# Kernel optimization log

Hardware: AMD Instinct MI355X
Metric: run time of the kernel (lower is better)

Reference implementation:

```python
import jax, jax.numpy as jnp
import numpy as np

G = 8192          # graphs in batch
A = 5             # num_agents (nodes per graph)
N = G * A         # total nodes
IN_CH = 29
HID = 64
HEADS = 8
D = HID * HEADS   # 512, node/graph feature dim
NOPT = 4
ADIM = 3


def _lin(key, fan_in, fan_out):
    return jax.random.normal(key, (fan_in, fan_out), jnp.float32) / np.sqrt(fan_in)


def setup_inputs() -> dict:
    key = jax.random.key(0)
    ks = jax.random.split(key, 40)
    # --- graph structure: G fully-connected 5-node graphs + self loops ---
    pairs = np.array([(i, j) for i in range(A) for j in range(A) if i != j])  # [20,2]
    base = (np.arange(G)[:, None] * A)
    src = (base + pairs[None, :, 0]).reshape(-1)
    dst = (base + pairs[None, :, 1]).reshape(-1)
    # GATConv adds self loops (fill_value=0.0 for edge_attr)
    loop = np.arange(N)
    edge_src = jnp.asarray(np.concatenate([src, loop]), jnp.int32)
    edge_dst = jnp.asarray(np.concatenate([dst, loop]), jnp.int32)
    e_real = jax.random.uniform(ks[0], (src.shape[0], 1), jnp.float32)
    edge_attr = jnp.concatenate([e_real, jnp.zeros((N, 1), jnp.float32)], axis=0)
    batch_map = jnp.asarray(np.repeat(np.arange(G), A), jnp.int32)
    x = jax.random.normal(ks[1], (N, IN_CH), jnp.float32)
    sc = 1.0 / np.sqrt(HID)
    inp = dict(
        x=x, edge_attr=edge_attr, edge_src=edge_src, edge_dst=edge_dst, batch_map=batch_map,
        # conv1
        W1=_lin(ks[2], IN_CH, D), as1=jax.random.normal(ks[3], (HEADS, HID)) * sc,
        ad1=jax.random.normal(ks[4], (HEADS, HID)) * sc, We1=_lin(ks[5], 1, D),
        ae1=jax.random.normal(ks[6], (HEADS, HID)) * sc, b1=jnp.zeros((D,), jnp.float32),
        # conv2
        W2=_lin(ks[7], D, D), as2=jax.random.normal(ks[8], (HEADS, HID)) * sc,
        ad2=jax.random.normal(ks[9], (HEADS, HID)) * sc, We2=_lin(ks[10], 1, D),
        ae2=jax.random.normal(ks[11], (HEADS, HID)) * sc, b2=jnp.zeros((D,), jnp.float32),
        # policy-over-options head
        pw1=_lin(ks[12], D, 2 * HID), pb1=jnp.zeros((2 * HID,)), pw2=_lin(ks[13], 2 * HID, NOPT), pb2=jnp.zeros((NOPT,)),
        # q-options head
        qw1=_lin(ks[14], D, 2 * HID), qb1=jnp.zeros((2 * HID,)), qw2=_lin(ks[15], 2 * HID, NOPT), qb2=jnp.zeros((NOPT,)),
        # intra-option actor head (option 0), input dim = node + graph feature = 2*D
        aw1=_lin(ks[16], 2 * D, 2 * HID), ab1=jnp.zeros((2 * HID,)), aw2=_lin(ks[17], 2 * HID, 2 * ADIM), ab2=jnp.zeros((2 * ADIM,)),
        # termination head (option 0)
        tw1=_lin(ks[18], D, HID), tb1=jnp.zeros((HID,)), tw2=_lin(ks[19], HID, 1), tb2=jnp.zeros((1,)),
        action_limits=jnp.array([1.0, 1.0, 3.14159], jnp.float32),
    )
    return inp


def _gat(x, src, dst, eattr, W, a_s, a_d, We, a_e, b):
    n = x.shape[0]
    h = (x @ W).reshape(n, HEADS, HID)                      # [N,H,C]
    e = (eattr @ We).reshape(-1, HEADS, HID)                # [E,H,C]
    lg = ((h * a_s).sum(-1)[src] + (h * a_d).sum(-1)[dst]
          + (e * a_e).sum(-1))                              # [E,H]
    lg = jnp.where(lg > 0, lg, 0.2 * lg)                    # leaky_relu(0.2)
    m = jax.ops.segment_max(lg, dst, num_segments=n)
    p = jnp.exp(lg - m[dst])
    denom = jax.ops.segment_sum(p, dst, num_segments=n)[dst] + 1e-16
    alpha = p / denom                                       # scatter-softmax over dst
    out = jax.ops.segment_sum(alpha[:, :, None] * h[src], dst, num_segments=n)
    return out.reshape(n, HEADS * HID) + b


def reference(x, edge_attr, edge_src, edge_dst, batch_map,
              W1, as1, ad1, We1, ae1, b1,
              W2, as2, ad2, We2, ae2, b2,
              pw1, pb1, pw2, pb2, qw1, qb1, qw2, qb2,
              aw1, ab1, aw2, ab2, tw1, tb1, tw2, tb2, action_limits):
    h = jax.nn.relu(_gat(x, edge_src, edge_dst, edge_attr, W1, as1, ad1, We1, ae1, b1))
    h = jax.nn.relu(_gat(h, edge_src, edge_dst, edge_attr, W2, as2, ad2, We2, ae2, b2))
    # global_mean_pool
    cnt = jax.ops.segment_sum(jnp.ones((h.shape[0],), h.dtype), batch_map, num_segments=G)
    g = jax.ops.segment_sum(h, batch_map, num_segments=G) / cnt[:, None]   # [G,D]
    pi = jax.nn.relu(g @ pw1 + pb1) @ pw2 + pb2                            # [G,NOPT]
    q = jax.nn.relu(g @ qw1 + qb1) @ qw2 + qb2                             # [G,NOPT]
    term = jax.nn.sigmoid(jax.nn.relu(g @ tw1 + tb1) @ tw2 + tb2)          # [G,1]
    # per-graph first num_agents nodes == all nodes here (5 per graph)
    agent = h.reshape(G, A, D)
    comb = jnp.concatenate([agent, jnp.broadcast_to(g[:, None, :], (G, A, D))], axis=-1)
    ho = jax.nn.relu(comb @ aw1 + ab1) @ aw2 + ab2                          # [G,A,6]
    mean_raw, log_std_raw = jnp.split(ho, 2, axis=-1)
    mean = jnp.tanh(mean_raw) * action_limits                               # [G,A,3]
    std = 0.05 + jax.nn.sigmoid(log_std_raw) * 0.45 + 1e-6
    return jnp.concatenate([pi, q, term, mean.reshape(G, -1), std.reshape(G, -1)], axis=1)
```

## Files before the change

### kernel.cpp

```cpp
#include <hip/hip_runtime.h>
#include <hip/hip_bf16.h>
#include <math.h>

#define GG 8192
#define AA 5
#define NN (GG * AA)
#define DD 512

typedef unsigned short ushort_t;
typedef unsigned int uint_t;

__device__ inline float bf2f(ushort_t u) {
  union { uint_t i; float f; } c; c.i = ((uint_t)u) << 16; return c.f;
}
__device__ inline ushort_t f2bf(float f) {
  union { float f; uint_t i; } c; c.f = f;
  uint_t r = c.i + 0x7fffu + ((c.i >> 16) & 1u);
  return (ushort_t)(r >> 16);
}

using frag8 = __attribute__((ext_vector_type(8))) short;
using f32x4 = __attribute__((ext_vector_type(4))) float;

typedef __attribute__((address_space(3))) void lds_void;
typedef __attribute__((address_space(1))) const void gbl_void;
#define GLL(g, l) __builtin_amdgcn_global_load_lds((gbl_void*)(g), (lds_void*)(l), 16, 0, 0)

__device__ inline int xcd_swz(int bid, int nwg) {
  return (bid & 7) * (nwg >> 3) + (bid >> 3);
}

__global__ __launch_bounds__(256) void k_prep(
    const float* __restrict__ x, const float* __restrict__ W1,
    const float* __restrict__ W2, const float* __restrict__ pw1,
    const float* __restrict__ qw1, const float* __restrict__ tw1,
    const float* __restrict__ aw1, const float* __restrict__ pb1,
    const float* __restrict__ qb1, const float* __restrict__ tb1,
    const float* __restrict__ ab1, const float* __restrict__ We1,
    const float* __restrict__ ae1, const float* __restrict__ We2,
    const float* __restrict__ ae2, const float* __restrict__ as1,
    const float* __restrict__ ad1, const float* __restrict__ as2,
    const float* __restrict__ ad2, const float* __restrict__ pw2,
    const float* __restrict__ pb2, const float* __restrict__ qw2,
    const float* __restrict__ qb2, const float* __restrict__ tw2,
    const float* __restrict__ tb2, const float* __restrict__ aw2,
    const float* __restrict__ ab2, ushort_t* __restrict__ xpad32,
    ushort_t* __restrict__ W1T32, ushort_t* __restrict__ W2T,
    ushort_t* __restrict__ WcatT, ushort_t* __restrict__ aw1topT,
    ushort_t* __restrict__ wsc1T, ushort_t* __restrict__ wsc2T,
    float* __restrict__ bcat, float* __restrict__ sce,
    float* __restrict__ woutT, float* __restrict__ bout) {
  int b = blockIdx.x;
  int t = threadIdx.x;
  if (b < 1024) {
    int i = b * 256 + t;
    int n = i >> 9, k = i & 511;
    W2T[(size_t)n * 512 + k] = f2bf(W2[(size_t)k * 512 + n]);
    float v;
    if (n < 128)      v = pw1[(size_t)k * 128 + n];
    else if (n < 256) v = qw1[(size_t)k * 128 + (n - 128)];
    else if (n < 320) v = tw1[(size_t)k * 64 + (n - 256)];
    else if (n < 448) v = aw1[(size_t)(512 + k) * 128 + (n - 320)];
    else              v = 0.f;
    WcatT[(size_t)n * 512 + k] = f2bf(v);
    if (n < 128) aw1topT[(size_t)n * 512 + k] = f2bf(aw1[(size_t)k * 128 + n]);
    if (k == 0) {
      float bv;
      if (n < 128)      bv = pb1[n];
      else if (n < 256) bv = qb1[n - 128];
      else if (n < 320) bv = tb1[n - 256];
      else if (n < 448) bv = ab1[n - 320];
      else              bv = 0.f;
      bcat[n] = bv;
    }
    if (i < 512 * 32) {
      int nn = i >> 5, kk = i & 31;
      W1T32[i] = (kk < 29) ? f2bf(W1[(size_t)kk * 512 + nn]) : (ushort_t)0;
    }
    if (i < 8192) {
      int k2 = i & 511, s = i >> 9;
      int head = s >> 1;
      const float* av = ((s & 1) ? ad2 : as2) + head * 64;
      const float* wr = W2 + (size_t)k2 * 512 + head * 64;
      float val = 0.f;
      for (int c = 0; c < 64; ++c) val = fmaf(wr[c], av[c], val);
      wsc2T[i] = f2bf(val);
    }
    if (i < 512) {
      int k1 = i & 31, s = i >> 5;
      int head = s >> 1;
      float val = 0.f;
      if (k1 < 29) {
        const float* av = ((s & 1) ? ad1 : as1) + head * 64;
        const float* wr = W1 + (size_t)k1 * 512 + head * 64;
        for (int c = 0; c < 64; ++c) val = fmaf(wr[c], av[c], val);
      }
      wsc1T[i] = f2bf(val);
    }
    if (i < 16) {
      int h = i & 7;
      const float* Wp = (i < 8) ? We1 : We2;
      const float* ap = (i < 8) ? ae1 : ae2;
      float c = 0.f;
      for (int k2 = 0; k2 < 64; ++k2) c = fmaf(Wp[h * 64 + k2], ap[h * 64 + k2], c);
      sce[i] = c;
    }
    if (i < 5120) {
      int j = i / 40, o = i % 40;
      float wv;
      if (o < 4)       wv = pw2[j * 4 + o];
      else if (o < 8)  wv = qw2[j * 4 + (o - 4)];
      else if (o == 8) wv = (j < 64) ? tw2[j] : 0.f;
      else if (o < 24) wv = aw2[j * 6 + (o - 9) % 3];
      else if (o < 39) wv = aw2[j * 6 + 3 + (o - 24) % 3];
      else             wv = 0.f;
      woutT[i] = wv;
      if (j == 0) {
        float bv;
        if (o < 4)       bv = pb2[o];
        else if (o < 8)  bv = qb2[o - 4];
        else if (o == 8) bv = tb2[0];
        else if (o < 24) bv = ab2[(o - 9) % 3];
        else if (o < 39) bv = ab2[3 + (o - 24) % 3];
        else             bv = 0.f;
        bout[o] = bv;
      }
    }
  } else {
    int i = (b - 1024) * 256 + t;
    int n = i >> 5, k = i & 31;
    xpad32[i] = (k < 29) ? f2bf(x[(size_t)n * 29 + k]) : (ushort_t)0;
  }
}

__global__ __launch_bounds__(1024) void k_mega(
    const ushort_t* __restrict__ xpad32, const ushort_t* __restrict__ W1T32,
    const ushort_t* __restrict__ wsc1T, const ushort_t* __restrict__ W2T,
    const ushort_t* __restrict__ wsc2T, const float* __restrict__ eattr,
    const float* __restrict__ sce, const float* __restrict__ b1,
    const float* __restrict__ b2, ushort_t* __restrict__ h2,
    ushort_t* __restrict__ gmean) {
  __shared__ __align__(16) char smem[149504];
  const int t = threadIdx.x;
  const int lane = t & 63;
  const int w = t >> 6;
  const int l15 = lane & 15;
  const int ko2 = ((((lane >> 4) ^ (lane & 3) ^ ((lane >> 2) & 3)) & 3) * 16);
  int lid = xcd_swz(blockIdx.x, gridDim.x);
  const int m0 = lid * 80;
  const int g0 = lid * 16;
  ushort_t* h1buf = (ushort_t*)smem;
  float* sal = (float*)(smem + 124160);
  float* sss = (float*)(smem + 136960);
  float* ssd = (float*)(smem + 139520);
  const f32x4 zz = {0.f, 0.f, 0.f, 0.f};
  f32x4 acc[5][2], asc[5];
#pragma unroll
  for (int mt = 0; mt < 5; ++mt) { acc[mt][0] = zz; acc[mt][1] = zz; asc[mt] = zz; }

  {
#pragma unroll
    for (int r_ = 0; r_ < 2; ++r_) {
      int c_ = t + r_ * 1024; int row_ = c_ >> 2;
      int sw_ = ((((c_ & 3) ^ (row_ & 3) ^ ((row_ >> 2) & 3)) & 3)) * 8;
      GLL(W1T32 + (size_t)row_ * 32 + sw_, smem + 81920 + c_ * 16);
    }
    if (t < 320) {
      int c_ = t; int row_ = c_ >> 2;
      int sw_ = ((((c_ & 3) ^ (row_ & 3) ^ ((row_ >> 2) & 3)) & 3)) * 8;
      GLL(xpad32 + (size_t)(m0 + row_) * 32 + sw_, smem + 114688 + c_ * 16);
    } else if (t < 384) {
      int c_ = t - 320; int row_ = c_ >> 2;
      int sw_ = ((((c_ & 3) ^ (row_ & 3) ^ ((row_ >> 2) & 3)) & 3)) * 8;
      GLL(wsc1T + (size_t)row_ * 32 + sw_, smem + 119808 + c_ * 16);
    }
  }
  asm volatile("s_waitcnt vmcnt(0)" ::: "memory");
  __builtin_amdgcn_s_barrier();
  {
    const char* bb = smem + 81920;
    const char* aa = smem + 114688;
    const char* sb = smem + 119808;
    frag8 af[5], bfr[2];
#pragma unroll
    for (int mt = 0; mt < 5; ++mt)
      af[mt] = *(const frag8*)(aa + (mt * 16 + l15) * 64 + ko2);
#pragma unroll
    for (int n = 0; n < 2; ++n)
      bfr[n] = *(const frag8*)(bb + ((2 * w + n) * 16 + l15) * 64 + ko2);
#pragma unroll
    for (int mt = 0; mt < 5; ++mt)
#pragma unroll
      for (int n = 0; n < 2; ++n)
        acc[mt][n] = __builtin_amdgcn_mfma_f32_16x16x32_bf16(af[mt], bfr[n], acc[mt][n], 0, 0, 0);
    if (w == 15) {
      frag8 sfr = *(const frag8*)(sb + l15 * 64 + ko2);
#pragma unroll
      for (int mt = 0; mt < 5; ++mt)
        asc[mt] = __builtin_amdgcn_mfma_f32_16x16x32_bf16(af[mt], sfr, asc[mt], 0, 0, 0);
    }
  }
  if (w == 15) {
    float* dst = (l15 & 1) ? ssd : sss;
    int hd = l15 >> 1;
    int q4 = (lane >> 4) * 4;
#pragma unroll
    for (int mt = 0; mt < 5; ++mt)
#pragma unroll
      for (int r = 0; r < 4; ++r)
        dst[(mt * 16 + q4 + r) * 8 + hd] = asc[mt][r];
  }
  __syncthreads();
  if (t < 640) {
    int gi = t / 40, jh = t % 40;
    int j = jh >> 3, hd = jh & 7;
    int g = g0 + gi;
    float sdj = ssd[(gi * 5 + j) * 8 + hd];
    float ce = sce[hd];
    float lg[5], mx = -1e30f;
#pragma unroll
    for (int i = 0; i < 5; ++i) {
      float l = sss[(gi * 5 + i) * 8 + hd] + sdj;
      if (i != j) l = fmaf(eattr[(size_t)g * 20 + i * 4 + (j > i ? j - 1 : j)], ce, l);
      l = l > 0.f ? l : 0.2f * l;
      lg[i] = l; mx = fmaxf(mx, l);
    }
    float s = 0.f;
#pragma unroll
    for (int i = 0; i < 5; ++i) { lg[i] = __expf(lg[i] - mx); s += lg[i]; }
    float inv = 1.f / (s + 1e-16f);
#pragma unroll
    for (int i = 0; i < 5; ++i) sal[((gi * 5 + j) * 5 + i) * 8 + hd] = lg[i] * inv;
  }
  __syncthreads();
  {
    float* hbf = (float*)(smem + 81920);
#pragma unroll
    for (int p = 0; p < 4; ++p) {
      if ((w >> 2) == p) {
        int q4 = (lane >> 4) * 4;
#pragma unroll
        for (int mt = 0; mt < 5; ++mt)
#pragma unroll
          for (int n = 0; n < 2; ++n) {
            int lc = (w & 3) * 32 + n * 16 + l15;
#pragma unroll
            for (int r = 0; r < 4; ++r)
              hbf[(mt * 16 + q4 + r) * 132 + lc] = acc[mt][n][r];
          }
      }
      __syncthreads();
      if (t < 512) {
        int gi = t >> 5, cq = t & 31;
        int hd = 2 * p + (cq >> 4);
        int cg = p * 128 + cq * 4;
        float hv[5][4];
#pragma unroll
        for (int i = 0; i < 5; ++i)
          *(float4*)hv[i] = *(const float4*)&hbf[(gi * 5 + i) * 132 + cq * 4];
        float4 bb4 = *(const float4*)&b1[cg];
        int chunk = cg >> 5, slot = (cg >> 3) & 3, boff = (cg & 7) * 2;
#pragma unroll
        for (int j = 0; j < 5; ++j) {
          float o0 = bb4.x, o1 = bb4.y, o2 = bb4.z, o3 = bb4.w;
#pragma unroll
          for (int i = 0; i < 5; ++i) {
            float a = sal[((gi * 5 + j) * 5 + i) * 8 + hd];
            o0 = fmaf(a, hv[i][0], o0); o1 = fmaf(a, hv[i][1], o1);
            o2 = fmaf(a, hv[i][2], o2); o3 = fmaf(a, hv[i][3], o3);
          }
          o0 = fmaxf(o0, 0.f); o1 = fmaxf(o1, 0.f);
          o2 = fmaxf(o2, 0.f); o3 = fmaxf(o3, 0.f);
          uint2 wv_;
          wv_.x = (uint_t)f2bf(o0) | ((uint_t)f2bf(o1) << 16);
          wv_.y = (uint_t)f2bf(o2) | ((uint_t)f2bf(o3) << 16);
          int row = gi * 5 + j;
          int phys = slot ^ (row & 3) ^ ((row >> 2) & 3);
          *(uint2*)((char*)h1buf + chunk * 5120 + row * 64 + phys * 16 + boff) = wv_;
        }
      }
      __syncthreads();
    }
  }

#pragma unroll
  for (int mt = 0; mt < 5; ++mt) { acc[mt][0] = zz; acc[mt][1] = zz; asc[mt] = zz; }
#define FS2(bi, kk0)                                                           \
  {                                                                            \
    char* bb_ = smem + 81920 + (bi) * 32768;                                   \
    char* sb_ = smem + 147456 + (bi) * 1024;                                   \
    _Pragma("unroll")                                                          \
    for (int r_ = 0; r_ < 2; ++r_) {                                           \
      int c_ = t + r_ * 1024; int row_ = c_ >> 2;                              \
      int sw_ = ((((c_ & 3) ^ (row_ & 3) ^ ((row_ >> 2) & 3)) & 3)) * 8;       \
      GLL(W2T + (size_t)row_ * 512 + (kk0) + sw_, bb_ + c_ * 16);              \
    }                                                                          \
    if (t < 64) {                                                              \
      int c_ = t; int row_ = c_ >> 2;                                          \
      int sw_ = ((((c_ & 3) ^ (row_ & 3) ^ ((row_ >> 2) & 3)) & 3)) * 8;       \
      GLL(wsc2T + (size_t)row_ * 512 + (kk0) + sw_, sb_ + c_ * 16);            \
    }                                                                          \
  }
  FS2(0, 0);
  asm volatile("s_waitcnt vmcnt(0)" ::: "memory");
  __builtin_amdgcn_s_barrier();
  for (int ts = 0; ts < 16; ++ts) {
    int cur = ts & 1;
    if (ts + 1 < 16) FS2(cur ^ 1, (ts + 1) * 32);
    const char* bb = smem + 81920 + cur * 32768;
    const char* aa = (const char*)h1buf + ts * 5120;
    const char* sb = smem + 147456 + cur * 1024;
    frag8 af[5], bfr[2];
#pragma unroll
    for (int mt = 0; mt < 5; ++mt)
      af[mt] = *(const frag8*)(aa + (mt * 16 + l15) * 64 + ko2);
#pragma unroll
    for (int n = 0; n < 2; ++n)
      bfr[n] = *(const frag8*)(bb + ((2 * w + n) * 16 + l15) * 64 + ko2);
    __builtin_amdgcn_s_setprio(1);
#pragma unroll
    for (int mt = 0; mt < 5; ++mt)
#pragma unroll
      for (int n = 0; n < 2; ++n)
        acc[mt][n] = __builtin_amdgcn_mfma_f32_16x16x32_bf16(af[mt], bfr[n], acc[mt][n], 0, 0, 0);
    if (w == 15) {
      frag8 sfr = *(const frag8*)(sb + l15 * 64 + ko2);
#pragma unroll
      for (int mt = 0; mt < 5; ++mt)
        asc[mt] = __builtin_amdgcn_mfma_f32_16x16x32_bf16(af[mt], sfr, asc[mt], 0, 0, 0);
    }
    __builtin_amdgcn_s_setprio(0);
    __builtin_amdgcn_sched_barrier(0);
    asm volatile("s_waitcnt vmcnt(0)" ::: "memory");
    __builtin_amdgcn_s_barrier();
  }
#undef FS2
  if (w == 15) {
    float* dst = (l15 & 1) ? ssd : sss;
    int hd = l15 >> 1;
    int q4 = (lane >> 4) * 4;
#pragma unroll
    for (int mt = 0; mt < 5; ++mt)
#pragma unroll
      for (int r = 0; r < 4; ++r)
        dst[(mt * 16 + q4 + r) * 8 + hd] = asc[mt][r];
  }
  __syncthreads();
  if (t < 640) {
    int gi = t / 40, jh = t % 40;
    int j = jh >> 3, hd = jh & 7;
    int g = g0 + gi;
    float sdj = ssd[(gi * 5 + j) * 8 + hd];
    float ce = sce[8 + hd];
    float lg[5], mx = -1e30f;
#pragma unroll
    for (int i = 0; i < 5; ++i) {
      float l = sss[(gi * 5 + i) * 8 + hd] + sdj;
      if (i != j) l = fmaf(eattr[(size_t)g * 20 + i * 4 + (j > i ? j - 1 : j)], ce, l);
      l = l > 0.f ? l : 0.2f * l;
      lg[i] = l; mx = fmaxf(mx, l);
    }
    float s = 0.f;
#pragma unroll
    for (int i = 0; i < 5; ++i) { lg[i] = __expf(lg[i] - mx); s += lg[i]; }
    float inv = 1.f / (s + 1e-16f);
#pragma unroll
    for (int i = 0; i < 5; ++i) sal[((gi * 5 + j) * 5 + i) * 8 + hd] = lg[i] * inv;
  }
  __syncthreads();
  {
    float* hbf = (float*)(smem + 81920);
#pragma unroll
    for (int p = 0; p < 4; ++p) {
      if ((w >> 2) == p) {
        int q4 = (lane >> 4) * 4;
#pragma unroll
        for (int mt = 0; mt < 5; ++mt)
#pragma unroll
          for (int n = 0; n < 2; ++n) {
            int lc = (w & 3) * 32 + n * 16 + l15;
#pragma unroll
            for (int r = 0; r < 4; ++r)
              hbf[(mt * 16 + q4 + r) * 132 + lc] = acc[mt][n][r];
          }
      }
      __syncthreads();
      if (t < 512) {
        int gi = t >> 5, cq = t & 31;
        int hd = 2 * p + (cq >> 4);
        int cg = p * 128 + cq * 4;
        float hv[5][4];
#pragma unroll
        for (int i = 0; i < 5; ++i)
          *(float4*)hv[i] = *(const float4*)&hbf[(gi * 5 + i) * 132 + cq * 4];
        float4 bb4 = *(const float4*)&b2[cg];
        float gs0 = 0.f, gs1 = 0.f, gs2 = 0.f, gs3 = 0.f;
#pragma unroll
        for (int j = 0; j < 5; ++j) {
          float o0 = bb4.x, o1 = bb4.y, o2 = bb4.z, o3 = bb4.w;
#pragma unroll
          for (int i = 0; i < 5; ++i) {
            float a = sal[((gi * 5 + j) * 5 + i) * 8 + hd];
            o0 = fmaf(a, hv[i][0], o0); o1 = fmaf(a, hv[i][1], o1);
            o2 = fmaf(a, hv[i][2], o2); o3 = fmaf(a, hv[i][3], o3);
          }
          o0 = fmaxf(o0, 0.f); o1 = fmaxf(o1, 0.f);
          o2 = fmaxf(o2, 0.f); o3 = fmaxf(o3, 0.f);
          uint2 wv_;
          wv_.x = (uint_t)f2bf(o0) | ((uint_t)f2bf(o1) << 16);
          wv_.y = (uint_t)f2bf(o2) | ((uint_t)f2bf(o3) << 16);
          *(uint2*)(h2 + ((size_t)(g0 + gi) * 5 + j) * 512 + cg) = wv_;
          gs0 += o0; gs1 += o1; gs2 += o2; gs3 += o3;
        }
        uint2 wv_;
        wv_.x = (uint_t)f2bf(gs0 * 0.2f) | ((uint_t)f2bf(gs1 * 0.2f) << 16);
        wv_.y = (uint_t)f2bf(gs2 * 0.2f) | ((uint_t)f2bf(gs3 * 0.2f) << 16);
        *(uint2*)(gmean + (size_t)(g0 + gi) * 512 + cg) = wv_;
      }
      __syncthreads();
    }
  }
}

template <int EPI>
__device__ __forceinline__ void gemm_body(
    const ushort_t* __restrict__ A, const ushort_t* __restrict__ BT,
    const float* __restrict__ bias, ushort_t* __restrict__ Cv,
    int M, int N, int K, int m0, int n0, char* lds) {
  int t = threadIdx.x;
  int lane = t & 63;
  int wv = t >> 6;
  int wr = (wv >> 1) * 64, wc = (wv & 1) * 64;
  f32x4 acc[4][4] = {};
  int ch0 = t, ch1 = t + 256;
  int row0 = ch0 >> 2, row1 = ch1 >> 2;
  int sw0 = (((ch0 & 3) ^ (row0 & 3) ^ ((row0 >> 2) & 3)) & 3) * 8;
  int sw1 = (((ch1 & 3) ^ (row1 & 3) ^ ((row1 >> 2) & 3)) & 3) * 8;
  int ko2 = ((((lane >> 4) ^ (lane & 3) ^ ((lane >> 2) & 3)) & 3) * 16);
  const int nt = K >> 5;
#define STAGE(bi, kk0)                                                         \
  {                                                                            \
    char* ab = lds + (bi) * 16384;                                             \
    GLL(A + (size_t)(m0 + row0) * K + (kk0) + sw0, ab + ch0 * 16);             \
    GLL(A + (size_t)(m0 + row1) * K + (kk0) + sw1, ab + ch1 * 16);             \
    GLL(BT + (size_t)(n0 + row0) * K + (kk0) + sw0, ab + 8192 + ch0 * 16);     \
    GLL(BT + (size_t)(n0 + row1) * K + (kk0) + sw1, ab + 8192 + ch1 * 16);     \
  }
  STAGE(0, 0);
  asm volatile("s_waitcnt vmcnt(0)" ::: "memory");
  __builtin_amdgcn_s_barrier();
  for (int ts = 0; ts < nt; ++ts) {
    int cur = ts & 1;
    if (ts + 1 < nt) STAGE(cur ^ 1, (ts + 1) * 32);
    const char* ab = lds + cur * 16384;
    frag8 af[4], bfr[4];
#pragma unroll
    for (int m = 0; m < 4; ++m)
      af[m] = *(const frag8*)(ab + (wr + m * 16 + (lane & 15)) * 64 + ko2);
#pragma unroll
    for (int n = 0; n < 4; ++n)
      bfr[n] = *(const frag8*)(ab + 8192 + (wc + n * 16 + (lane & 15)) * 64 + ko2);
    __builtin_amdgcn_s_setprio(1);
#pragma unroll
    for (int m = 0; m < 4; ++m)
#pragma unroll
      for (int n = 0; n < 4; ++n)
        acc[m][n] = __builtin_amdgcn_mfma_f32_16x16x32_bf16(af[m], bfr[n], acc[m][n], 0, 0, 0);
    __builtin_amdgcn_s_setprio(0);
    __builtin_amdgcn_sched_barrier(0);
    asm volatile("s_waitcnt vmcnt(0)" ::: "memory");
    __builtin_amdgcn_s_barrier();
  }
#undef STAGE
  int r4 = (lane >> 4) * 4;
  int cl = lane & 15;
#pragma unroll
  for (int m = 0; m < 4; ++m) {
#pragma unroll
    for (int n = 0; n < 4; ++n) {
      int col = n0 + wc + n * 16 + cl;
      float bb = (EPI == 2) ? bias[col] : 0.f;
#pragma unroll
      for (int r = 0; r < 4; ++r) {
        int row = m0 + wr + m * 16 + r4 + r;
        float v = acc[m][n][r] + bb;
        if (EPI == 2 && col < 320) v = fmaxf(v, 0.f);
        Cv[(size_t)row * N + col] = f2bf(v);
      }
    }
  }
}

__global__ __launch_bounds__(256) void k_hgemm(
    const ushort_t* __restrict__ h2, const ushort_t* __restrict__ aw1topT,
    ushort_t* __restrict__ ahid, const ushort_t* __restrict__ gmean,
    const ushort_t* __restrict__ WcatT, const float* __restrict__ bcat,
    ushort_t* __restrict__ hcat) {
  __shared__ char lds[32768];
  int bid = blockIdx.x;
  if (bid < 320) {
    int lid = xcd_swz(bid, 320);
    gemm_body<1>(h2, aw1topT, nullptr, ahid, NN, 128, DD, lid * 128, 0, lds);
  } else {
    int lid = xcd_swz(bid - 320, 256);
    gemm_body<2>(gmean, WcatT, bcat, hcat, GG, DD, DD, (lid >> 2) * 128, (lid & 3) * 128, lds);
  }
}

__global__ __launch_bounds__(256) void k_heads(
    const ushort_t* __restrict__ hcat, const ushort_t* __restrict__ ahid,
    const float* __restrict__ woutT, const float* __restrict__ bout,
    const float* __restrict__ alim, float* __restrict__ out) {
  int g0 = blockIdx.x * 4;
  int t = threadIdx.x;
  __shared__ float sbuf[4224];
  for (int i = t; i < 4224; i += 256) {
    int gi = i / 1056, r = i - gi * 1056;
    const ushort_t* grow = hcat + (size_t)(g0 + gi) * 512;
    float v = 0.f;
    if (r < 128)                  v = bf2f(grow[r]);
    else if (r >= 132 && r < 260) v = bf2f(grow[128 + r - 132]);
    else if (r >= 264 && r < 328) v = bf2f(grow[256 + r - 264]);
    else if (r >= 396) {
      int q = r - 396; int a = q / 132; int j = q - a * 132;
      if (j < 128)
        v = fmaxf(bf2f(ahid[((size_t)(g0 + gi) * 5 + a) * 128 + j]) + bf2f(grow[320 + j]), 0.f);
    }
    sbuf[i] = v;
  }
  __syncthreads();
  int gi = t >> 6, o = t & 63;
  int oc = o < 39 ? o : 39;
  int seg;
  if (oc < 4)       seg = 0;
  else if (oc < 8)  seg = 132;
  else if (oc == 8) seg = 264;
  else {
    int idx = (oc < 24) ? oc - 9 : oc - 24;
    seg = 396 + (idx / 3) * 132;
  }
  const float* ip = &sbuf[gi * 1056 + seg];
  float a0 = 0.f, a1 = 0.f, a2 = 0.f, a3 = 0.f;
#pragma unroll
  for (int j = 0; j < 128; j += 4) {
    a0 = fmaf(ip[j + 0], woutT[(j + 0) * 40 + oc], a0);
    a1 = fmaf(ip[j + 1], woutT[(j + 1) * 40 + oc], a1);
    a2 = fmaf(ip[j + 2], woutT[(j + 2) * 40 + oc], a2);
    a3 = fmaf(ip[j + 3], woutT[(j + 3) * 40 + oc], a3);
  }
  float res = (a0 + a1) + (a2 + a3) + bout[oc];
  if (o < 39) {
    if (o == 8)       res = 1.f / (1.f + __expf(-res));
    else if (o >= 24) res = 0.05f + 0.45f / (1.f + __expf(-res)) + 1e-6f;
    else if (o >= 9)  res = tanhf(res) * alim[(o - 9) % 3];
    out[(size_t)(g0 + gi) * 39 + o] = res;
  }
}

extern "C" void kernel_launch(void* const* d_in, const int* in_sizes, int n_in,
                              void* d_out, int out_size, void* d_ws, size_t ws_size,
                              hipStream_t stream) {
  const float* x     = (const float*)d_in[0];
  const float* eattr = (const float*)d_in[1];
  const float* W1  = (const float*)d_in[5];
  const float* as1 = (const float*)d_in[6];
  const float* ad1 = (const float*)d_in[7];
  const float* We1 = (const float*)d_in[8];
  const float* ae1 = (const float*)d_in[9];
  const float* b1  = (const float*)d_in[10];
  const float* W2  = (const float*)d_in[11];
  const float* as2 = (const float*)d_in[12];
  const float* ad2 = (const float*)d_in[13];
  const float* We2 = (const float*)d_in[14];
  const float* ae2 = (const float*)d_in[15];
  const float* b2  = (const float*)d_in[16];
  const float* pw1 = (const float*)d_in[17];
  const float* pb1 = (const float*)d_in[18];
  const float* pw2 = (const float*)d_in[19];
  const float* pb2 = (const float*)d_in[20];
  const float* qw1 = (const float*)d_in[21];
  const float* qb1 = (const float*)d_in[22];
  const float* qw2 = (const float*)d_in[23];
  const float* qb2 = (const float*)d_in[24];
  const float* aw1 = (const float*)d_in[25];
  const float* ab1 = (const float*)d_in[26];
  const float* aw2 = (const float*)d_in[27];
  const float* ab2 = (const float*)d_in[28];
  const float* tw1 = (const float*)d_in[29];
  const float* tb1 = (const float*)d_in[30];
  const float* tw2 = (const float*)d_in[31];
  const float* tb2 = (const float*)d_in[32];
  const float* alim = (const float*)d_in[33];

  const size_t BIGE = (size_t)NN * DD;
  char* p = (char*)d_ws;
  ushort_t* h2     = (ushort_t*)p; p += BIGE * 2;
  ushort_t* gmean  = (ushort_t*)p; p += (size_t)GG * DD * 2;
  ushort_t* xpad32 = (ushort_t*)p; p += (size_t)NN * 32 * 2;
  ushort_t* W1T32  = (ushort_t*)p; p += (size_t)512 * 32 * 2;
  ushort_t* W2T    = (ushort_t*)p; p += (size_t)512 * 512 * 2;
  ushort_t* WcatT  = (ushort_t*)p; p += (size_t)512 * 512 * 2;
  ushort_t* aw1topT = (ushort_t*)p; p += (size_t)128 * 512 * 2;
  ushort_t* wsc1T  = (ushort_t*)p; p += (size_t)16 * 32 * 2;
  ushort_t* wsc2T  = (ushort_t*)p; p += (size_t)16 * 512 * 2;
  float* bcat  = (float*)p; p += 512 * 4;
  float* sce   = (float*)p; p += 16 * 4;
  float* woutT = (float*)p; p += 5120 * 4;
  float* bout  = (float*)p; p += 40 * 4;
  ushort_t* ahid = (ushort_t*)p; p += (size_t)NN * 128 * 2;
  ushort_t* hcat = (ushort_t*)p;

  k_prep<<<1024 + 5120, 256, 0, stream>>>(
      x, W1, W2, pw1, qw1, tw1, aw1, pb1, qb1, tb1, ab1,
      We1, ae1, We2, ae2, as1, ad1, as2, ad2,
      pw2, pb2, qw2, qb2, tw2, tb2, aw2, ab2,
      xpad32, W1T32, W2T, WcatT, aw1topT, wsc1T, wsc2T,
      bcat, sce, woutT, bout);
  k_mega<<<GG / 16, 1024, 0, stream>>>(
      xpad32, W1T32, wsc1T, W2T, wsc2T, eattr, sce, b1, b2, h2, gmean);
  k_hgemm<<<320 + 256, 256, 0, stream>>>(h2, aw1topT, ahid, gmean, WcatT, bcat, hcat);
  k_heads<<<GG / 4, 256, 0, stream>>>(hcat, ahid, woutT, bout, alim, (float*)d_out);
}
```

Measured before the change: 105.8 us.

## Fuse head GEMMs into mega kernel, keep h2 and gmean in LDS

The second-layer GAT output and per-graph mean now stay in shared memory instead of being written to global h2/gmean buffers. The actor-hidden GEMM (h2 × aw1top) and the concatenated head GEMM (gmean × Wcat) run inside k_mega on that on-chip data, and the separate k_hgemm launch is removed. This avoids a roughly 40 MB round trip through global memory plus one kernel launch. In exchange each block does extra small GEMMs with poorly shaped tiles (16-row gmean tile, uneven 3/2 m-tile split), restages the weights per block, and uses more LDS.

```diff
diff --git a/kernel.cpp b/kernel.cpp
--- a/kernel.cpp
+++ b/kernel.cpp
@@ -136,11 +136,12 @@
 __global__ __launch_bounds__(1024) void k_mega(
     const ushort_t* __restrict__ xpad32, const ushort_t* __restrict__ W1T32,
     const ushort_t* __restrict__ wsc1T, const ushort_t* __restrict__ W2T,
-    const ushort_t* __restrict__ wsc2T, const float* __restrict__ eattr,
-    const float* __restrict__ sce, const float* __restrict__ b1,
-    const float* __restrict__ b2, ushort_t* __restrict__ h2,
-    ushort_t* __restrict__ gmean) {
-  __shared__ __align__(16) char smem[149504];
+    const ushort_t* __restrict__ wsc2T, const ushort_t* __restrict__ aw1topT,
+    const ushort_t* __restrict__ WcatT, const float* __restrict__ bcat,
+    const float* __restrict__ eattr, const float* __restrict__ sce,
+    const float* __restrict__ b1, const float* __restrict__ b2,
+    ushort_t* __restrict__ ahid, ushort_t* __restrict__ hcat) {
+  __shared__ __align__(16) char smem[158720];
   const int t = threadIdx.x;
   const int lane = t & 63;
   const int w = t >> 6;
@@ -149,10 +150,11 @@
   int lid = xcd_swz(blockIdx.x, gridDim.x);
   const int m0 = lid * 80;
   const int g0 = lid * 16;
-  ushort_t* h1buf = (ushort_t*)smem;
+  ushort_t* hbuf = (ushort_t*)smem;
   float* sal = (float*)(smem + 124160);
   float* sss = (float*)(smem + 136960);
   float* ssd = (float*)(smem + 139520);
+  ushort_t* gmb = (ushort_t*)(smem + 142080);
   const f32x4 zz = {0.f, 0.f, 0.f, 0.f};
   f32x4 acc[5][2], asc[5];
 #pragma unroll
@@ -276,7 +278,7 @@
           wv_.y = (uint_t)f2bf(o2) | ((uint_t)f2bf(o3) << 16);
           int row = gi * 5 + j;
           int phys = slot ^ (row & 3) ^ ((row >> 2) & 3);
-          *(uint2*)((char*)h1buf + chunk * 5120 + row * 64 + phys * 16 + boff) = wv_;
+          *(uint2*)((char*)hbuf + chunk * 5120 + row * 64 + phys * 16 + boff) = wv_;
         }
       }
       __syncthreads();
@@ -308,7 +310,7 @@
     int cur = ts & 1;
     if (ts + 1 < 16) FS2(cur ^ 1, (ts + 1) * 32);
     const char* bb = smem + 81920 + cur * 32768;
-    const char* aa = (const char*)h1buf + ts * 5120;
+    const char* aa = (const char*)hbuf + ts * 5120;
     const char* sb = smem + 147456 + cur * 1024;
     frag8 af[5], bfr[2];
 #pragma unroll
@@ -394,6 +396,7 @@
         for (int i = 0; i < 5; ++i)
           *(float4*)hv[i] = *(const float4*)&hbf[(gi * 5 + i) * 132 + cq * 4];
         float4 bb4 = *(const float4*)&b2[cg];
+        int chunk = cg >> 5, slot = (cg >> 3) & 3, boff = (cg & 7) * 2;
         float gs0 = 0.f, gs1 = 0.f, gs2 = 0.f, gs3 = 0.f;
 #pragma unroll
         for (int j = 0; j < 5; ++j) {
@@ -409,101 +412,117 @@
           uint2 wv_;
           wv_.x = (uint_t)f2bf(o0) | ((uint_t)f2bf(o1) << 16);
           wv_.y = (uint_t)f2bf(o2) | ((uint_t)f2bf(o3) << 16);
-          *(uint2*)(h2 + ((size_t)(g0 + gi) * 5 + j) * 512 + cg) = wv_;
+          int row = gi * 5 + j;
+          int phys = slot ^ (row & 3) ^ ((row >> 2) & 3);
+          *(uint2*)((char*)hbuf + chunk * 5120 + row * 64 + phys * 16 + boff) = wv_;
           gs0 += o0; gs1 += o1; gs2 += o2; gs3 += o3;
         }
-        uint2 wv_;
-        wv_.x = (uint_t)f2bf(gs0 * 0.2f) | ((uint_t)f2bf(gs1 * 0.2f) << 16);
-        wv_.y = (uint_t)f2bf(gs2 * 0.2f) | ((uint_t)f2bf(gs3 * 0.2f) << 16);
-        *(uint2*)(gmean + (size_t)(g0 + gi) * 512 + cg) = wv_;
+        uint2 gv_;
+        gv_.x = (uint_t)f2bf(gs0 * 0.2f) | ((uint_t)f2bf(gs1 * 0.2f) << 16);
+        gv_.y = (uint_t)f2bf(gs2 * 0.2f) | ((uint_t)f2bf(gs3 * 0.2f) << 16);
+        *(uint2*)(gmb + (size_t)gi * 520 + cg) = gv_;
       }
       __syncthreads();
     }
   }
-}
-
-template <int EPI>
-__device__ __forceinline__ void gemm_body(
-    const ushort_t* __restrict__ A, const ushort_t* __restrict__ BT,
-    const float* __restrict__ bias, ushort_t* __restrict__ Cv,
-    int M, int N, int K, int m0, int n0, char* lds) {
-  int t = threadIdx.x;
-  int lane = t & 63;
-  int wv = t >> 6;
-  int wr = (wv >> 1) * 64, wc = (wv & 1) * 64;
-  f32x4 acc[4][4] = {};
-  int ch0 = t, ch1 = t + 256;
-  int row0 = ch0 >> 2, row1 = ch1 >> 2;
-  int sw0 = (((ch0 & 3) ^ (row0 & 3) ^ ((row0 >> 2) & 3)) & 3) * 8;
-  int sw1 = (((ch1 & 3) ^ (row1 & 3) ^ ((row1 >> 2) & 3)) & 3) * 8;
-  int ko2 = ((((lane >> 4) ^ (lane & 3) ^ ((lane >> 2) & 3)) & 3) * 16);
-  const int nt = K >> 5;
-#define STAGE(bi, kk0)                                                         \
-  {                                                                            \
-    char* ab = lds + (bi) * 16384;                                             \
-    GLL(A + (size_t)(m0 + row0) * K + (kk0) + sw0, ab + ch0 * 16);             \
-    GLL(A + (size_t)(m0 + row1) * K + (kk0) + sw1, ab + ch1 * 16);             \
-    GLL(BT + (size_t)(n0 + row0) * K + (kk0) + sw0, ab + 8192 + ch0 * 16);     \
-    GLL(BT + (size_t)(n0 + row1) * K + (kk0) + sw1, ab + 8192 + ch1 * 16);     \
-  }
-  STAGE(0, 0);
-  asm volatile("s_waitcnt vmcnt(0)" ::: "memory");
-  __builtin_amdgcn_s_barrier();
-  for (int ts = 0; ts < nt; ++ts) {
-    int cur = ts & 1;
-    if (ts + 1 < nt) STAGE(cur ^ 1, (ts + 1) * 32);
-    const char* ab = lds + cur * 16384;
-    frag8 af[4], bfr[4];
-#pragma unroll
-    for (int m = 0; m < 4; ++m)
-      af[m] = *(const frag8*)(ab + (wr + m * 16 + (lane & 15)) * 64 + ko2);
-#pragma unroll
-    for (int n = 0; n < 4; ++n)
-      bfr[n] = *(const frag8*)(ab + 8192 + (wc + n * 16 + (lane & 15)) * 64 + ko2);
-    __builtin_amdgcn_s_setprio(1);
-#pragma unroll
-    for (int m = 0; m < 4; ++m)
-#pragma unroll
-      for (int n = 0; n < 4; ++n)
-        acc[m][n] = __builtin_amdgcn_mfma_f32_16x16x32_bf16(af[m], bfr[n], acc[m][n], 0, 0, 0);
-    __builtin_amdgcn_s_setprio(0);
-    __builtin_amdgcn_sched_barrier(0);
+
+  {
+    f32x4 acc3[3] = {zz, zz, zz};
+    const int ntile = w >> 1;
+    const int mg = w & 1;
+    const int mtb = mg ? 3 : 0;
+    const int nmt = mg ? 2 : 3;
+#define FS3A(bi, kk0)                                                          \
+    if (t < 512) {                                                             \
+      char* bb_ = smem + 81920 + (bi) * 8192;                                  \
+      int c_ = t; int row_ = c_ >> 2;                                          \
+      int sw_ = ((((c_ & 3) ^ (row_ & 3) ^ ((row_ >> 2) & 3)) & 3)) * 8;       \
+      GLL(aw1topT + (size_t)row_ * 512 + (kk0) + sw_, bb_ + c_ * 16);          \
+    }
+    FS3A(0, 0);
     asm volatile("s_waitcnt vmcnt(0)" ::: "memory");
     __builtin_amdgcn_s_barrier();
-  }
-#undef STAGE
-  int r4 = (lane >> 4) * 4;
-  int cl = lane & 15;
-#pragma unroll
-  for (int m = 0; m < 4; ++m) {
-#pragma unroll
-    for (int n = 0; n < 4; ++n) {
-      int col = n0 + wc + n * 16 + cl;
-      float bb = (EPI == 2) ? bias[col] : 0.f;
+    for (int ts = 0; ts < 16; ++ts) {
+      int cur = ts & 1;
+      if (ts + 1 < 16) FS3A(cur ^ 1, (ts + 1) * 32);
+      const char* bb = smem + 81920 + cur * 8192;
+      const char* aa = (const char*)hbuf + ts * 5120;
+      frag8 bfr = *(const frag8*)(bb + (ntile * 16 + l15) * 64 + ko2);
+      frag8 af[3];
+#pragma unroll
+      for (int q = 0; q < 3; ++q)
+        if (q < nmt)
+          af[q] = *(const frag8*)(aa + ((mtb + q) * 16 + l15) * 64 + ko2);
+      __builtin_amdgcn_s_setprio(1);
+#pragma unroll
+      for (int q = 0; q < 3; ++q)
+        if (q < nmt)
+          acc3[q] = __builtin_amdgcn_mfma_f32_16x16x32_bf16(af[q], bfr, acc3[q], 0, 0, 0);
+      __builtin_amdgcn_s_setprio(0);
+      __builtin_amdgcn_sched_barrier(0);
+      asm volatile("s_waitcnt vmcnt(0)" ::: "memory");
+      __builtin_amdgcn_s_barrier();
+    }
+#undef FS3A
+    int q4 = (lane >> 4) * 4;
+#pragma unroll
+    for (int q = 0; q < 3; ++q)
+      if (q < nmt) {
+#pragma unroll
+        for (int r = 0; r < 4; ++r) {
+          int row = m0 + (mtb + q) * 16 + q4 + r;
+          ahid[(size_t)row * 128 + ntile * 16 + l15] = f2bf(acc3[q][r]);
+        }
+      }
+  }
+
+  {
+    f32x4 acc3[2] = {zz, zz};
+#define FS3B(bi, kk0)                                                          \
+    {                                                                          \
+      char* bb_ = smem + (bi) * 32768;                                         \
+      _Pragma("unroll")                                                        \
+      for (int r_ = 0; r_ < 2; ++r_) {                                         \
+        int c_ = t + r_ * 1024; int row_ = c_ >> 2;                            \
+        int sw_ = ((((c_ & 3) ^ (row_ & 3) ^ ((row_ >> 2) & 3)) & 3)) * 8;     \
+        GLL(WcatT + (size_t)row_ * 512 + (kk0) + sw_, bb_ + c_ * 16);          \
+      }                                                                        \
+    }
+    FS3B(0, 0);
+    asm volatile("s_waitcnt vmcnt(0)" ::: "memory");
+    __builtin_amdgcn_s_barrier();
+    for (int ts = 0; ts < 16; ++ts) {
+      int cur = ts & 1;
+      if (ts + 1 < 16) FS3B(cur ^ 1, (ts + 1) * 32);
+      const char* bb = smem + cur * 32768;
+      frag8 afr = *(const frag8*)((const char*)gmb + (size_t)l15 * 1040 + ts * 64 + (lane >> 4) * 16);
+      frag8 bfr[2];
+#pragma unroll
+      for (int n = 0; n < 2; ++n)
+        bfr[n] = *(const frag8*)(bb + ((2 * w + n) * 16 + l15) * 64 + ko2);
+      __builtin_amdgcn_s_setprio(1);
+#pragma unroll
+      for (int n = 0; n < 2; ++n)
+        acc3[n] = __builtin_amdgcn_mfma_f32_16x16x32_bf16(afr, bfr[n], acc3[n], 0, 0, 0);
+      __builtin_amdgcn_s_setprio(0);
+      __builtin_amdgcn_sched_barrier(0);
+      asm volatile("s_waitcnt vmcnt(0)" ::: "memory");
+      __builtin_amdgcn_s_barrier();
+    }
+#undef FS3B
+    int q4 = (lane >> 4) * 4;
+#pragma unroll
+    for (int n = 0; n < 2; ++n) {
+      int col = (2 * w + n) * 16 + l15;
+      float bc = bcat[col];
 #pragma unroll
       for (int r = 0; r < 4; ++r) {
-        int row = m0 + wr + m * 16 + r4 + r;
-        float v = acc[m][n][r] + bb;
-        if (EPI == 2 && col < 320) v = fmaxf(v, 0.f);
-        Cv[(size_t)row * N + col] = f2bf(v);
-      }
-    }
-  }
-}
-
-__global__ __launch_bounds__(256) void k_hgemm(
-    const ushort_t* __restrict__ h2, const ushort_t* __restrict__ aw1topT,
-    ushort_t* __restrict__ ahid, const ushort_t* __restrict__ gmean,
-    const ushort_t* __restrict__ WcatT, const float* __restrict__ bcat,
-    ushort_t* __restrict__ hcat) {
-  __shared__ char lds[32768];
-  int bid = blockIdx.x;
-  if (bid < 320) {
-    int lid = xcd_swz(bid, 320);
-    gemm_body<1>(h2, aw1topT, nullptr, ahid, NN, 128, DD, lid * 128, 0, lds);
-  } else {
-    int lid = xcd_swz(bid - 320, 256);
-    gemm_body<2>(gmean, WcatT, bcat, hcat, GG, DD, DD, (lid >> 2) * 128, (lid & 3) * 128, lds);
+        int gi = q4 + r;
+        float v = acc3[n][r] + bc;
+        if (col < 320) v = fmaxf(v, 0.f);
+        hcat[(size_t)(g0 + gi) * 512 + col] = f2bf(v);
+      }
+    }
   }
 }
 
@@ -592,10 +611,7 @@
   const float* tb2 = (const float*)d_in[32];
   const float* alim = (const float*)d_in[33];
 
-  const size_t BIGE = (size_t)NN * DD;
   char* p = (char*)d_ws;
-  ushort_t* h2     = (ushort_t*)p; p += BIGE * 2;
-  ushort_t* gmean  = (ushort_t*)p; p += (size_t)GG * DD * 2;
   ushort_t* xpad32 = (ushort_t*)p; p += (size_t)NN * 32 * 2;
   ushort_t* W1T32  = (ushort_t*)p; p += (size_t)512 * 32 * 2;
   ushort_t* W2T    = (ushort_t*)p; p += (size_t)512 * 512 * 2;
@@ -617,7 +633,7 @@
       xpad32, W1T32, W2T, WcatT, aw1topT, wsc1T, wsc2T,
       bcat, sce, woutT, bout);
   k_mega<<<GG / 16, 1024, 0, stream>>>(
-      xpad32, W1T32, wsc1T, W2T, wsc2T, eattr, sce, b1, b2, h2, gmean);
-  k_hgemm<<<320 + 256, 256, 0, stream>>>(h2, aw1topT, ahid, gmean, WcatT, bcat, hcat);
+      xpad32, W1T32, wsc1T, W2T, wsc2T, aw1topT, WcatT, bcat,
+      eattr, sce, b1, b2, ahid, hcat);
   k_heads<<<GG / 4, 256, 0, stream>>>(hcat, ahid, woutT, bout, alim, (float*)d_out);
 }
```

Result: slower. 130.8 us (+23.7%).
